# Kernel tuning notes

Measured on AMD Instinct MI355X. Metric: run time of the kernel, lower is better.

Reference implementation:

```python
import jax, jax.numpy as jnp
import numpy as np

B, I, H = 8192, 1024, 1024

def _xavier(key, out_f, in_f):
    limit = (6.0 / (in_f + out_f)) ** 0.5
    return jax.random.uniform(key, (out_f, in_f), jnp.float32, -limit, limit)

def setup_inputs() -> dict:
    key = jax.random.key(0)
    ks = jax.random.split(key, 11)
    inp = {
        'x': jax.random.normal(ks[0], (B, I), jnp.float32),
        'h': jax.random.normal(ks[1], (B, H), jnp.float32),
        'c': jax.random.normal(ks[2], (B, H), jnp.float32),
    }
    names = ['Wxi', 'Whi', 'Wxf', 'Whf', 'Wxo', 'Who', 'Wxg', 'Whg']
    for n, k in zip(names, ks[3:]):
        in_f = I if n[1] == 'x' else H
        inp[n + '_w'] = _xavier(k, H, in_f)
        inp[n + '_b'] = jnp.zeros((H,), jnp.float32)
    return inp

def reference(x, h, c,
              Wxi_w, Wxi_b, Whi_w, Whi_b,
              Wxf_w, Wxf_b, Whf_w, Whf_b,
              Wxo_w, Wxo_b, Who_w, Who_b,
              Wxg_w, Wxg_b, Whg_w, Whg_b):
    Wx = jnp.concatenate([Wxi_w, Wxf_w, Wxo_w, Wxg_w], axis=0)  # [4H, I]
    Wh = jnp.concatenate([Whi_w, Whf_w, Who_w, Whg_w], axis=0)  # [4H, H]
    bx = jnp.concatenate([Wxi_b, Wxf_b, Wxo_b, Wxg_b], axis=0)  # [4H]
    bh = jnp.concatenate([Whi_b, Whf_b, Who_b, Whg_b], axis=0)  # [4H]
    z = x @ Wx.T + bx + h @ Wh.T + bh  # [B, 4H]
    zi, zf, zo, zg = jnp.split(z, 4, axis=-1)
    it = jax.nn.sigmoid(zi)
    ft = jax.nn.sigmoid(zf)
    ot = jax.nn.sigmoid(zo)
    gt = jnp.tanh(zg)
    c_next = ft * c + it * gt
    h_next = ot * jnp.tanh(c_next)
    return (h_next, c_next)
```

## Files before the change

kernel.cpp:

```cpp
#include <hip/hip_runtime.h>
#include <hip/hip_bf16.h>
#include <cstdint>


typedef __bf16 bf16;
typedef __attribute__((ext_vector_type(8))) bf16 bf16x8;
typedef __attribute__((ext_vector_type(4))) float f32x4;

#define CN_OFF 8388608

__global__ __launch_bounds__(256) void pack_all(
    const float* __restrict__ x, const float* __restrict__ h,
    const float* __restrict__ wxi, const float* __restrict__ whi,
    const float* __restrict__ wxf, const float* __restrict__ whf,
    const float* __restrict__ wxo, const float* __restrict__ who,
    const float* __restrict__ wxg, const float* __restrict__ whg,
    const float* __restrict__ bxi, const float* __restrict__ bhi,
    const float* __restrict__ bxf, const float* __restrict__ bhf,
    const float* __restrict__ bxo, const float* __restrict__ bho,
    const float* __restrict__ bxg, const float* __restrict__ bhg,
    bf16* __restrict__ A2, bf16* __restrict__ B2, float* __restrict__ Bcomb) {
  int b = blockIdx.x;
  if (b < 8192) {
    int chunk = b * 256 + threadIdx.x;
    int lane = chunk & 63;
    int mi   = (chunk >> 6) & 3;
    int wm   = (chunk >> 8) & 1;
    int kt   = (chunk >> 9) & 63;
    int mb   = chunk >> 15;
    int m = mb * 128 + wm * 64 + mi * 16 + (lane & 15);
    int k = kt * 32 + (lane >> 4) * 8;
    const float* src = (k < 1024) ? (x + (size_t)m * 1024 + k)
                                  : (h + (size_t)m * 1024 + (k - 1024));
    f32x4 v0 = *(const f32x4*)src;
    f32x4 v1 = *(const f32x4*)(src + 4);
    bf16x8 o;
    o[0]=(bf16)v0[0]; o[1]=(bf16)v0[1]; o[2]=(bf16)v0[2]; o[3]=(bf16)v0[3];
    o[4]=(bf16)v1[0]; o[5]=(bf16)v1[1]; o[6]=(bf16)v1[2]; o[7]=(bf16)v1[3];
    *(bf16x8*)(A2 + (size_t)chunk * 8) = o;
  } else {
    int chunk = (b - 8192) * 256 + threadIdx.x;
    int lane = chunk & 63;
    int gate = (chunk >> 6) & 3;
    int wn   = (chunk >> 8) & 1;
    int kt   = (chunk >> 9) & 63;
    int nb   = chunk >> 15;
    int jl = lane & 15;
    int j  = (nb * 2 + wn) * 16 + jl;
    int k  = kt * 32 + (lane >> 4) * 8;
    const float* wx = (gate == 0) ? wxi : (gate == 1) ? wxf : (gate == 2) ? wxo : wxg;
    const float* wh = (gate == 0) ? whi : (gate == 1) ? whf : (gate == 2) ? who : whg;
    const float* src = (k < 1024) ? (wx + (size_t)j * 1024 + k)
                                  : (wh + (size_t)j * 1024 + (k - 1024));
    f32x4 v0 = *(const f32x4*)src;
    f32x4 v1 = *(const f32x4*)(src + 4);
    bf16x8 o;
    o[0]=(bf16)v0[0]; o[1]=(bf16)v0[1]; o[2]=(bf16)v0[2]; o[3]=(bf16)v0[3];
    o[4]=(bf16)v1[0]; o[5]=(bf16)v1[1]; o[6]=(bf16)v1[2]; o[7]=(bf16)v1[3];
    *(bf16x8*)(B2 + (size_t)chunk * 8) = o;
    if (kt == 0 && (lane >> 4) == 0) {
      const float* bx = (gate == 0) ? bxi : (gate == 1) ? bxf : (gate == 2) ? bxo : bxg;
      const float* bh = (gate == 0) ? bhi : (gate == 1) ? bhf : (gate == 2) ? bho : bhg;
      Bcomb[(nb * 2 + wn) * 64 + gate * 16 + jl] = bx[j] + bh[j];
    }
  }
}

__device__ __forceinline__ float sigf(float v) { return 1.f / (1.f + __expf(-v)); }
__device__ __forceinline__ float tanhfast(float v) {
  v = fminf(15.f, fmaxf(-15.f, v));
  float e = __expf(2.f * v);
  return (e - 1.f) / (e + 1.f);
}

__global__ __launch_bounds__(256) void gemm_lstm(const bf16* __restrict__ A2,
                                                 const bf16* __restrict__ B2,
                                                 const float* __restrict__ Bcomb,
                                                 const float* __restrict__ c,
                                                 float* __restrict__ out) {
  const int t    = threadIdx.x;
  const int wave = t >> 6;
  const int lane = t & 63;
  const int nb = blockIdx.x;
  const int mb = blockIdx.y;
  const int wm = wave >> 1;
  const int wn = wave & 1;
  const int lrow = lane & 15;
  const int lkg  = lane >> 4;

  const bf16* pa = A2 + (size_t)mb * 262144 + wm * 2048 + lane * 8;
  const bf16* pb = B2 + (size_t)nb * 262144 + wn * 2048 + lane * 8;

  f32x4 acc[4][4] = {};
  bf16x8 a0[4], b0[4], a1[4], b1[4];

#pragma unroll
  for (int i = 0; i < 4; ++i) {
    a0[i] = *(const bf16x8*)(pa + i * 512);
    b0[i] = *(const bf16x8*)(pb + i * 512);
  }
#pragma unroll
  for (int i = 0; i < 4; ++i) {
    a1[i] = *(const bf16x8*)(pa + 4096 + i * 512);
    b1[i] = *(const bf16x8*)(pb + 4096 + i * 512);
  }

  for (int kt = 0; kt < 64; kt += 2) {
#pragma unroll
    for (int mi = 0; mi < 4; ++mi)
#pragma unroll
      for (int ni = 0; ni < 4; ++ni)
        acc[mi][ni] = __builtin_amdgcn_mfma_f32_16x16x32_bf16(a0[mi], b0[ni], acc[mi][ni], 0, 0, 0);
    if (kt + 2 < 64) {
      const bf16* qa = pa + (size_t)(kt + 2) * 4096;
      const bf16* qb = pb + (size_t)(kt + 2) * 4096;
#pragma unroll
      for (int i = 0; i < 4; ++i) {
        a0[i] = *(const bf16x8*)(qa + i * 512);
        b0[i] = *(const bf16x8*)(qb + i * 512);
      }
    }
#pragma unroll
    for (int mi = 0; mi < 4; ++mi)
#pragma unroll
      for (int ni = 0; ni < 4; ++ni)
        acc[mi][ni] = __builtin_amdgcn_mfma_f32_16x16x32_bf16(a1[mi], b1[ni], acc[mi][ni], 0, 0, 0);
    if (kt + 3 < 64) {
      const bf16* qa = pa + (size_t)(kt + 3) * 4096;
      const bf16* qb = pb + (size_t)(kt + 3) * 4096;
#pragma unroll
      for (int i = 0; i < 4; ++i) {
        a1[i] = *(const bf16x8*)(qa + i * 512);
        b1[i] = *(const bf16x8*)(qb + i * 512);
      }
    }
  }

  const int jg = (nb * 2 + wn) * 16 + lrow;
  const int bbase = (nb * 2 + wn) * 64 + lrow;
  const float bi  = Bcomb[bbase +  0];
  const float bf_ = Bcomb[bbase + 16];
  const float bo  = Bcomb[bbase + 32];
  const float bg  = Bcomb[bbase + 48];

#pragma unroll
  for (int mi = 0; mi < 4; ++mi) {
    const int row0 = mb * 128 + wm * 64 + mi * 16 + lkg * 4;
    float cv[4];
#pragma unroll
    for (int r = 0; r < 4; ++r)
      cv[r] = c[(size_t)(row0 + r) * 1024 + jg];
#pragma unroll
    for (int r = 0; r < 4; ++r) {
      float zi = acc[mi][0][r] + bi;
      float zf = acc[mi][1][r] + bf_;
      float zo = acc[mi][2][r] + bo;
      float zg = acc[mi][3][r] + bg;
      float it = sigf(zi), ft = sigf(zf), ot = sigf(zo), gt = tanhfast(zg);
      float cn = ft * cv[r] + it * gt;
      size_t off = (size_t)(row0 + r) * 1024 + jg;
      out[off] = ot * tanhfast(cn);
      out[CN_OFF + off] = cn;
    }
  }
}

extern "C" void kernel_launch(void* const* d_in, const int* in_sizes, int n_in,
                              void* d_out, int out_size, void* d_ws, size_t ws_size,
                              hipStream_t stream) {
  const float* x   = (const float*)d_in[0];
  const float* h   = (const float*)d_in[1];
  const float* c   = (const float*)d_in[2];
  const float* Wxi = (const float*)d_in[3];  const float* bxi = (const float*)d_in[4];
  const float* Whi = (const float*)d_in[5];  const float* bhi = (const float*)d_in[6];
  const float* Wxf = (const float*)d_in[7];  const float* bxf = (const float*)d_in[8];
  const float* Whf = (const float*)d_in[9];  const float* bhf = (const float*)d_in[10];
  const float* Wxo = (const float*)d_in[11]; const float* bxo = (const float*)d_in[12];
  const float* Who = (const float*)d_in[13]; const float* bho = (const float*)d_in[14];
  const float* Wxg = (const float*)d_in[15]; const float* bxg = (const float*)d_in[16];
  const float* Whg = (const float*)d_in[17]; const float* bhg = (const float*)d_in[18];
  float* out = (float*)d_out;

  bf16*  Abuf  = (bf16*)d_ws;
  bf16*  Wbuf  = Abuf + (size_t)8192 * 2048;
  float* Bcomb = (float*)(Wbuf + (size_t)4096 * 2048);

  pack_all<<<12288, 256, 0, stream>>>(x, h,
                                      Wxi, Whi, Wxf, Whf, Wxo, Who, Wxg, Whg,
                                      bxi, bhi, bxf, bhf, bxo, bho, bxg, bhg,
                                      Abuf, Wbuf, Bcomb);
  gemm_lstm<<<dim3(32, 64), 256, 0, stream>>>(Abuf, Wbuf, Bcomb, c, out);
}
```

Baseline: 359.0 us.

## Stage GEMM tiles through LDS with double buffering and larger block tiles

The GEMM moves from 128x128 tiles loaded straight into registers per wave to 256x256 block tiles (512 threads) staged into LDS with global_load_lds and double buffering. Waves now share A and B fragments, which cuts global and L2 traffic. Block IDs are remapped so tiles on the same XCD share B columns, and MFMA priority is raised around the compute. The pack kernel is also rewritten to read coalesced rows through a swizzled LDS transpose. The cost is 128KB of LDS per block and heavier register pressure (8x4 accumulators), which limits occupancy.

```diff
diff --git a/kernel.cpp b/kernel.cpp
--- a/kernel.cpp
+++ b/kernel.cpp
@@ -8,6 +8,19 @@
 typedef __attribute__((ext_vector_type(4))) float f32x4;
 
 #define CN_OFF 8388608
+
+__device__ __forceinline__ void gload16(const bf16* g, bf16* l) {
+  __builtin_amdgcn_global_load_lds(
+      (const __attribute__((address_space(1))) void*)g,
+      (__attribute__((address_space(3))) void*)l, 16, 0, 0);
+}
+
+__device__ __forceinline__ bf16x8 cvt8(f32x4 v0, f32x4 v1) {
+  bf16x8 o;
+  o[0]=(bf16)v0[0]; o[1]=(bf16)v0[1]; o[2]=(bf16)v0[2]; o[3]=(bf16)v0[3];
+  o[4]=(bf16)v1[0]; o[5]=(bf16)v1[1]; o[6]=(bf16)v1[2]; o[7]=(bf16)v1[3];
+  return o;
+}
 
 __global__ __launch_bounds__(256) void pack_all(
     const float* __restrict__ x, const float* __restrict__ h,
@@ -20,48 +33,79 @@
     const float* __restrict__ bxo, const float* __restrict__ bho,
     const float* __restrict__ bxg, const float* __restrict__ bhg,
     bf16* __restrict__ A2, bf16* __restrict__ B2, float* __restrict__ Bcomb) {
-  int b = blockIdx.x;
-  if (b < 8192) {
-    int chunk = b * 256 + threadIdx.x;
-    int lane = chunk & 63;
-    int mi   = (chunk >> 6) & 3;
-    int wm   = (chunk >> 8) & 1;
-    int kt   = (chunk >> 9) & 63;
-    int mb   = chunk >> 15;
-    int m = mb * 128 + wm * 64 + mi * 16 + (lane & 15);
-    int k = kt * 32 + (lane >> 4) * 8;
-    const float* src = (k < 1024) ? (x + (size_t)m * 1024 + k)
-                                  : (h + (size_t)m * 1024 + (k - 1024));
-    f32x4 v0 = *(const f32x4*)src;
-    f32x4 v1 = *(const f32x4*)(src + 4);
-    bf16x8 o;
-    o[0]=(bf16)v0[0]; o[1]=(bf16)v0[1]; o[2]=(bf16)v0[2]; o[3]=(bf16)v0[3];
-    o[4]=(bf16)v1[0]; o[5]=(bf16)v1[1]; o[6]=(bf16)v1[2]; o[7]=(bf16)v1[3];
-    *(bf16x8*)(A2 + (size_t)chunk * 8) = o;
+  __shared__ __align__(16) bf16 lds[8192];
+  const int t = threadIdx.x;
+  const int bid = blockIdx.x;
+
+  if (bid < 2048) {
+    const int mb = bid >> 5;
+    const int wm = (bid >> 4) & 1;
+    const int q  = bid & 15;
+    const int rowbase = mb * 128 + wm * 64;
+    const float* srcM; int k0;
+    if (q < 8) { srcM = x; k0 = q * 128; } else { srcM = h; k0 = q * 128 - 1024; }
+#pragma unroll
+    for (int r = 0; r < 4; ++r) {
+      const int rl = r * 16 + (t >> 4);
+      const int cc = (t & 15) * 8;
+      const float* s = srcM + (size_t)(rowbase + rl) * 1024 + k0 + cc;
+      f32x4 v0 = *(const f32x4*)s;
+      f32x4 v1 = *(const f32x4*)(s + 4);
+      const int chunkS = (t & 15) ^ (rl & 7);
+      *(bf16x8*)((char*)lds + rl * 256 + chunkS * 16) = cvt8(v0, v1);
+    }
+    __syncthreads();
+#pragma unroll
+    for (int r = 0; r < 4; ++r) {
+      const int idx = r * 256 + t;
+      const int fj  = idx >> 6;
+      const int ktL = fj >> 2, mi = fj & 3;
+      const int l   = idx & 63;
+      const int srow = mi * 16 + (l & 15);
+      const int chunkS = (ktL * 4 + (l >> 4)) ^ (srow & 7);
+      bf16x8 o = *(const bf16x8*)((const char*)lds + srow * 256 + chunkS * 16);
+      size_t el = ((size_t)mb * 64 + q * 4 + ktL) * 4096 + (size_t)wm * 2048 + mi * 512 + l * 8;
+      *(bf16x8*)(A2 + el) = o;
+    }
   } else {
-    int chunk = (b - 8192) * 256 + threadIdx.x;
-    int lane = chunk & 63;
-    int gate = (chunk >> 6) & 3;
-    int wn   = (chunk >> 8) & 1;
-    int kt   = (chunk >> 9) & 63;
-    int nb   = chunk >> 15;
-    int jl = lane & 15;
-    int j  = (nb * 2 + wn) * 16 + jl;
-    int k  = kt * 32 + (lane >> 4) * 8;
-    const float* wx = (gate == 0) ? wxi : (gate == 1) ? wxf : (gate == 2) ? wxo : wxg;
-    const float* wh = (gate == 0) ? whi : (gate == 1) ? whf : (gate == 2) ? who : whg;
-    const float* src = (k < 1024) ? (wx + (size_t)j * 1024 + k)
-                                  : (wh + (size_t)j * 1024 + (k - 1024));
-    f32x4 v0 = *(const f32x4*)src;
-    f32x4 v1 = *(const f32x4*)(src + 4);
-    bf16x8 o;
-    o[0]=(bf16)v0[0]; o[1]=(bf16)v0[1]; o[2]=(bf16)v0[2]; o[3]=(bf16)v0[3];
-    o[4]=(bf16)v1[0]; o[5]=(bf16)v1[1]; o[6]=(bf16)v1[2]; o[7]=(bf16)v1[3];
-    *(bf16x8*)(B2 + (size_t)chunk * 8) = o;
-    if (kt == 0 && (lane >> 4) == 0) {
-      const float* bx = (gate == 0) ? bxi : (gate == 1) ? bxf : (gate == 2) ? bxo : bxg;
-      const float* bh = (gate == 0) ? bhi : (gate == 1) ? bhf : (gate == 2) ? bho : bhg;
-      Bcomb[(nb * 2 + wn) * 64 + gate * 16 + jl] = bx[j] + bh[j];
+    const int bid2 = bid - 2048;
+    const int nb   = bid2 >> 6;
+    const int gate = (bid2 >> 4) & 3;
+    const int q    = bid2 & 15;
+    const float* wxm = (gate == 0) ? wxi : (gate == 1) ? wxf : (gate == 2) ? wxo : wxg;
+    const float* whm = (gate == 0) ? whi : (gate == 1) ? whf : (gate == 2) ? who : whg;
+    const float* srcM; int k0;
+    if (q < 8) { srcM = wxm; k0 = q * 128; } else { srcM = whm; k0 = q * 128 - 1024; }
+    const int jbase = nb * 32;
+#pragma unroll
+    for (int r = 0; r < 2; ++r) {
+      const int rl = r * 16 + (t >> 4);
+      const int cc = (t & 15) * 8;
+      const float* s = srcM + (size_t)(jbase + rl) * 1024 + k0 + cc;
+      f32x4 v0 = *(const f32x4*)s;
+      f32x4 v1 = *(const f32x4*)(s + 4);
+      const int chunkS = (t & 15) ^ (rl & 7);
+      *(bf16x8*)((char*)lds + rl * 256 + chunkS * 16) = cvt8(v0, v1);
+    }
+    __syncthreads();
+#pragma unroll
+    for (int r = 0; r < 2; ++r) {
+      const int idx = r * 256 + t;
+      const int fj  = idx >> 6;
+      const int ktL = fj >> 1, wn = fj & 1;
+      const int l   = idx & 63;
+      const int srow = wn * 16 + (l & 15);
+      const int chunkS = (ktL * 4 + (l >> 4)) ^ (srow & 7);
+      bf16x8 o = *(const bf16x8*)((const char*)lds + srow * 256 + chunkS * 16);
+      size_t el = ((size_t)nb * 64 + q * 4 + ktL) * 4096 + (size_t)wn * 2048 + gate * 512 + l * 8;
+      *(bf16x8*)(B2 + el) = o;
+    }
+    if (q == 0 && t < 32) {
+      const float* bxv = (gate == 0) ? bxi : (gate == 1) ? bxf : (gate == 2) ? bxo : bxg;
+      const float* bhv = (gate == 0) ? bhi : (gate == 1) ? bhf : (gate == 2) ? bho : bhg;
+      const int wn = t >> 4, jl = t & 15;
+      const int j = nb * 32 + wn * 16 + jl;
+      Bcomb[(nb * 2 + wn) * 64 + gate * 16 + jl] = bxv[j] + bhv[j];
     }
   }
 }
@@ -73,69 +117,82 @@
   return (e - 1.f) / (e + 1.f);
 }
 
-__global__ __launch_bounds__(256) void gemm_lstm(const bf16* __restrict__ A2,
-                                                 const bf16* __restrict__ B2,
-                                                 const float* __restrict__ Bcomb,
-                                                 const float* __restrict__ c,
-                                                 float* __restrict__ out) {
+__global__ __launch_bounds__(512, 2) void gemm_lstm(const bf16* __restrict__ A2,
+                                                    const bf16* __restrict__ B2,
+                                                    const float* __restrict__ Bcomb,
+                                                    const float* __restrict__ c,
+                                                    float* __restrict__ out) {
+  __shared__ __align__(16) bf16 lds[65536];
   const int t    = threadIdx.x;
   const int wave = t >> 6;
   const int lane = t & 63;
-  const int nb = blockIdx.x;
-  const int mb = blockIdx.y;
-  const int wm = wave >> 1;
-  const int wn = wave & 1;
-  const int lrow = lane & 15;
-  const int lkg  = lane >> 4;
-
-  const bf16* pa = A2 + (size_t)mb * 262144 + wm * 2048 + lane * 8;
-  const bf16* pb = B2 + (size_t)nb * 262144 + wn * 2048 + lane * 8;
-
-  f32x4 acc[4][4] = {};
-  bf16x8 a0[4], b0[4], a1[4], b1[4];
-
-#pragma unroll
-  for (int i = 0; i < 4; ++i) {
-    a0[i] = *(const bf16x8*)(pa + i * 512);
-    b0[i] = *(const bf16x8*)(pb + i * 512);
+
+  const int bid = blockIdx.x;
+  const int xcd = bid & 7;
+  const int idx = bid >> 3;
+  const int bn  = xcd * 2 + (idx & 1);
+  const int bm  = idx >> 1;
+
+  const int wr  = wave >> 2;
+  const int wc  = wave & 3;
+  const int nbL = wc >> 1, wn = wc & 1;
+  const int lrow = lane & 15, lkg = lane >> 4;
+
+  const int tEl = t * 8;
+  const int wEl = (t & ~63) * 8;
+
+  const bf16* aSrc0 = A2 + (size_t)(2 * bm)     * 64 * 4096;
+  const bf16* aSrc1 = A2 + (size_t)(2 * bm + 1) * 64 * 4096;
+  const bf16* bSrc0 = B2 + (size_t)(2 * bn)     * 64 * 4096;
+  const bf16* bSrc1 = B2 + (size_t)(2 * bn + 1) * 64 * 4096;
+
+  auto stage = [&](int tile, int buf) {
+    const size_t kOff = (size_t)tile * 8192;
+    bf16* d = lds + buf * 32768;
+    const bf16* s0 = aSrc0 + kOff;
+    const bf16* s1 = aSrc1 + kOff;
+    const bf16* s2 = bSrc0 + kOff;
+    const bf16* s3 = bSrc1 + kOff;
+#pragma unroll
+    for (int hh = 0; hh < 2; ++hh) {
+      gload16(s0 + hh * 4096 + tEl, d +         hh * 4096 + wEl);
+      gload16(s1 + hh * 4096 + tEl, d +  8192 + hh * 4096 + wEl);
+      gload16(s2 + hh * 4096 + tEl, d + 16384 + hh * 4096 + wEl);
+      gload16(s3 + hh * 4096 + tEl, d + 24576 + hh * 4096 + wEl);
+    }
+  };
+
+  f32x4 acc[8][4] = {};
+
+  stage(0, 0);
+  __syncthreads();
+
+  for (int kt2 = 0; kt2 < 32; ++kt2) {
+    const int p = kt2 & 1;
+    if (kt2 + 1 < 32) stage(kt2 + 1, p ^ 1);
+    const bf16* bufA = lds + p * 32768 + wr * 8192;
+    const bf16* bufB = lds + p * 32768 + 16384 + nbL * 8192 + wn * 2048;
+#pragma unroll
+    for (int ktL = 0; ktL < 2; ++ktL) {
+      bf16x8 af[8], bfr[4];
+#pragma unroll
+      for (int i = 0; i < 8; ++i)
+        af[i] = *(const bf16x8*)(bufA + ktL * 4096 + i * 512 + lane * 8);
+#pragma unroll
+      for (int g = 0; g < 4; ++g)
+        bfr[g] = *(const bf16x8*)(bufB + ktL * 4096 + g * 512 + lane * 8);
+      __builtin_amdgcn_s_setprio(1);
+#pragma unroll
+      for (int i = 0; i < 8; ++i)
+#pragma unroll
+        for (int g = 0; g < 4; ++g)
+          acc[i][g] = __builtin_amdgcn_mfma_f32_16x16x32_bf16(af[i], bfr[g], acc[i][g], 0, 0, 0);
+      __builtin_amdgcn_s_setprio(0);
+    }
+    __syncthreads();
   }
-#pragma unroll
-  for (int i = 0; i < 4; ++i) {
-    a1[i] = *(const bf16x8*)(pa + 4096 + i * 512);
-    b1[i] = *(const bf16x8*)(pb + 4096 + i * 512);
-  }
-
-  for (int kt = 0; kt < 64; kt += 2) {
-#pragma unroll
-    for (int mi = 0; mi < 4; ++mi)
-#pragma unroll
-      for (int ni = 0; ni < 4; ++ni)
-        acc[mi][ni] = __builtin_amdgcn_mfma_f32_16x16x32_bf16(a0[mi], b0[ni], acc[mi][ni], 0, 0, 0);
-    if (kt + 2 < 64) {
-      const bf16* qa = pa + (size_t)(kt + 2) * 4096;
-      const bf16* qb = pb + (size_t)(kt + 2) * 4096;
-#pragma unroll
-      for (int i = 0; i < 4; ++i) {
-        a0[i] = *(const bf16x8*)(qa + i * 512);
-        b0[i] = *(const bf16x8*)(qb + i * 512);
-      }
-    }
-#pragma unroll
-    for (int mi = 0; mi < 4; ++mi)
-#pragma unroll
-      for (int ni = 0; ni < 4; ++ni)
-        acc[mi][ni] = __builtin_amdgcn_mfma_f32_16x16x32_bf16(a1[mi], b1[ni], acc[mi][ni], 0, 0, 0);
-    if (kt + 3 < 64) {
-      const bf16* qa = pa + (size_t)(kt + 3) * 4096;
-      const bf16* qb = pb + (size_t)(kt + 3) * 4096;
-#pragma unroll
-      for (int i = 0; i < 4; ++i) {
-        a1[i] = *(const bf16x8*)(qa + i * 512);
-        b1[i] = *(const bf16x8*)(qb + i * 512);
-      }
-    }
-  }
-
+
+  const int nb = bn * 2 + nbL;
   const int jg = (nb * 2 + wn) * 16 + lrow;
   const int bbase = (nb * 2 + wn) * 64 + lrow;
   const float bi  = Bcomb[bbase +  0];
@@ -144,18 +201,18 @@
   const float bg  = Bcomb[bbase + 48];
 
 #pragma unroll
-  for (int mi = 0; mi < 4; ++mi) {
-    const int row0 = mb * 128 + wm * 64 + mi * 16 + lkg * 4;
+  for (int i = 0; i < 8; ++i) {
+    const int row0 = (2 * bm + wr) * 128 + (i >> 2) * 64 + (i & 3) * 16 + lkg * 4;
     float cv[4];
 #pragma unroll
     for (int r = 0; r < 4; ++r)
       cv[r] = c[(size_t)(row0 + r) * 1024 + jg];
 #pragma unroll
     for (int r = 0; r < 4; ++r) {
-      float zi = acc[mi][0][r] + bi;
-      float zf = acc[mi][1][r] + bf_;
-      float zo = acc[mi][2][r] + bo;
-      float zg = acc[mi][3][r] + bg;
+      float zi = acc[i][0][r] + bi;
+      float zf = acc[i][1][r] + bf_;
+      float zo = acc[i][2][r] + bo;
+      float zg = acc[i][3][r] + bg;
       float it = sigf(zi), ft = sigf(zf), ot = sigf(zo), gt = tanhfast(zg);
       float cn = ft * cv[r] + it * gt;
       size_t off = (size_t)(row0 + r) * 1024 + jg;
@@ -185,9 +242,9 @@
   bf16*  Wbuf  = Abuf + (size_t)8192 * 2048;
   float* Bcomb = (float*)(Wbuf + (size_t)4096 * 2048);
 
-  pack_all<<<12288, 256, 0, stream>>>(x, h,
-                                      Wxi, Whi, Wxf, Whf, Wxo, Who, Wxg, Whg,
-                                      bxi, bhi, bxf, bhf, bxo, bho, bxg, bhg,
-                                      Abuf, Wbuf, Bcomb);
-  gemm_lstm<<<dim3(32, 64), 256, 0, stream>>>(Abuf, Wbuf, Bcomb, c, out);
-}
+  pack_all<<<4096, 256, 0, stream>>>(x, h,
+                                     Wxi, Whi, Wxf, Whf, Wxo, Who, Wxg, Whg,
+                                     bxi, bhi, bxf, bhf, bxo, bho, bxg, bhg,
+                                     Abuf, Wbuf, Bcomb);
+  gemm_lstm<<<512, 512, 0, stream>>>(Abuf, Wbuf, Bcomb, c, out);
+}
```

New measurement: 316.9 us. 11.7% less time.
